# Kernel tuning notes

Hardware: AMD Instinct MI355X
Metric: run time of the kernel (lower is better)

## Reference

```python
import jax, jax.numpy as jnp
import numpy as np

DIM = 96
NUM_HEADS = 6
KSIZE = 3
DILATIONS = (1, 2, 3)
HEAD_DIM = DIM // NUM_HEADS            # 16
NUM_DIL = len(DILATIONS)
GROUP_DIM = DIM // NUM_DIL             # 32 channels per dilation branch
MLP_HIDDEN = int(DIM * 4.0)
SCALE = HEAD_DIM ** -0.5
EPS = 1e-5


def _unfold(x, k, dil):
    """nn.Unfold(k, dilation=dil, padding=dil*(k-1)//2, stride=1).
    x: (B, C, H, W) -> (B, C, k*k, H, W), kernel positions row-major."""
    B, C, H, W = x.shape
    pad = dil * (k - 1) // 2
    xp = jnp.pad(x, ((0, 0), (0, 0), (pad, pad), (pad, pad)))
    pats = [xp[:, :, i * dil:i * dil + H, j * dil:j * dil + W]
            for i in range(k) for j in range(k)]
    return jnp.stack(pats, axis=2)  # (B, C, kk, H, W)


def _layernorm(x, w, b):
    mu = jnp.mean(x, axis=-1, keepdims=True)
    var = jnp.mean(jnp.square(x - mu), axis=-1, keepdims=True)
    return (x - mu) * jax.lax.rsqrt(var + EPS) * w + b


def _dilate_attention(q, k, v, dil):
    """q,k,v: (B, GROUP_DIM, H, W) -> (B, H, W, GROUP_DIM)."""
    B, gd, H, W = q.shape
    h = gd // HEAD_DIM
    kk = KSIZE * KSIZE
    HW = H * W
    qf = q.reshape(B, h, HEAD_DIM, HW)                      # bhdn
    ku = _unfold(k, KSIZE, dil).reshape(B, h, HEAD_DIM, kk, HW)  # bhdkn
    attn = jnp.einsum('bhdn,bhdkn->bhnk', qf, ku) * SCALE   # (B,h,HW,kk)
    attn = jax.nn.softmax(attn, axis=-1)
    vu = _unfold(v, KSIZE, dil).reshape(B, h, HEAD_DIM, kk, HW)
    out = jnp.einsum('bhnk,bhdkn->bnhd', attn, vu)          # (B,HW,h,HEAD_DIM)
    return out.reshape(B, H, W, gd)


def setup_inputs() -> dict:
    key = jax.random.key(0)
    ks = jax.random.split(key, 8)
    B, H, W = 8, 128, 128
    s = 0.02
    return {
        'x': jax.random.normal(ks[0], (B, DIM, H, W), jnp.float32),
        'qkv_w': jax.random.normal(ks[1], (3 * DIM, DIM), jnp.float32) * s,
        'proj_w': jax.random.normal(ks[2], (DIM, DIM), jnp.float32) * s,
        'proj_b': jnp.zeros((DIM,), jnp.float32),
        'ln1_w': jnp.ones((DIM,), jnp.float32),
        'ln1_b': jnp.zeros((DIM,), jnp.float32),
        'ln2_w': jnp.ones((DIM,), jnp.float32),
        'ln2_b': jnp.zeros((DIM,), jnp.float32),
        'fc1_w': jax.random.normal(ks[3], (MLP_HIDDEN, DIM), jnp.float32) * s,
        'fc1_b': jnp.zeros((MLP_HIDDEN,), jnp.float32),
        'fc2_w': jax.random.normal(ks[4], (DIM, MLP_HIDDEN), jnp.float32) * s,
        'fc2_b': jnp.zeros((DIM,), jnp.float32),
    }


def reference(x, qkv_w, proj_w, proj_b, ln1_w, ln1_b, ln2_w, ln2_b,
              fc1_w, fc1_b, fc2_w, fc2_b):
    B, C, H, W = x.shape
    xhw = jnp.transpose(x, (0, 2, 3, 1))                    # (B,H,W,C)

    # --- attention branch ---
    y = _layernorm(xhw, ln1_w, ln1_b)                       # (B,H,W,C)
    # qkv 1x1 conv == per-pixel matmul; output channel layout (3, nd, gd)
    qkv = jnp.einsum('bhwc,oc->bohw', y, qkv_w)             # (B,3C,H,W)
    qkv = qkv.reshape(B, 3, NUM_DIL, GROUP_DIM, H, W)
    outs = [
        _dilate_attention(qkv[:, 0, i], qkv[:, 1, i], qkv[:, 2, i], DILATIONS[i])
        for i in range(NUM_DIL)
    ]
    attn_out = jnp.concatenate(outs, axis=-1)               # (B,H,W,C)
    attn_out = jnp.einsum('bhwc,oc->bhwo', attn_out, proj_w) + proj_b
    xhw = xhw + attn_out

    # --- MLP branch ---
    y = _layernorm(xhw, ln2_w, ln2_b)
    h1 = jax.nn.gelu(jnp.einsum('bhwc,oc->bhwo', y, fc1_w) + fc1_b,
                     approximate=False)
    mlp_out = jnp.einsum('bhwc,oc->bhwo', h1, fc2_w) + fc2_b
    xhw = xhw + mlp_out

    return jnp.transpose(xhw, (0, 3, 1, 2))                 # (B,C,H,W)
```

## Files before the change

### kernel.cpp

```cpp
#include <hip/hip_runtime.h>
#include <hip/hip_bf16.h>
#include <math.h>

typedef __attribute__((ext_vector_type(8))) short bf16x8;
typedef __attribute__((ext_vector_type(4))) float f32x4;
typedef __attribute__((ext_vector_type(2))) unsigned u32x2;

#define MTOT  131072
#define HW16K 16384

__device__ inline float bf2f(unsigned short u) {
    union { unsigned u; float f; } x; x.u = ((unsigned)u) << 16; return x.f;
}
__device__ inline unsigned short f2bf(float a) {
    __hip_bfloat16 h = __float2bfloat16(a);
    union { __hip_bfloat16 h; unsigned short u; } c; c.h = h; return c.u;
}
__device__ inline unsigned pack2bf(float a, float b) {
    __hip_bfloat162 h = __float22bfloat162_rn(make_float2(a, b));
    union { __hip_bfloat162 h; unsigned u; } c; c.h = h; return c.u;
}
__device__ inline float gelu(float v) {
    float u = v * fmaf(0.07135481f, v * v, 1.5957691f);
    return __fdividef(v, 1.f + __expf(-u));
}
__device__ inline void load16(const unsigned short* p, float* f) {
    uint4 u0 = *(const uint4*)p;
    uint4 u1 = *(const uint4*)(p + 8);
    unsigned w[8] = {u0.x, u0.y, u0.z, u0.w, u1.x, u1.y, u1.z, u1.w};
#pragma unroll
    for (int i = 0; i < 8; i++) {
        union { unsigned u; float f; } lo, hi;
        lo.u = w[i] << 16; hi.u = w[i] & 0xffff0000u;
        f[2 * i] = lo.f; f[2 * i + 1] = hi.f;
    }
}

__global__ __launch_bounds__(256) void k_prep(const float* __restrict__ qw,
                                              const float* __restrict__ pw,
                                              const float* __restrict__ f1,
                                              const float* __restrict__ f2,
                                              unsigned short* __restrict__ wq,
                                              unsigned short* __restrict__ wp,
                                              unsigned short* __restrict__ w1t,
                                              unsigned short* __restrict__ w2t) {
    int t = blockIdx.x * 256 + threadIdx.x;
    if (t < 27648) {
        int row = t / 96, col = t - row * 96;
        int s = row / 96;
        int rem = row - s * 96;
        int di = rem >> 5;
        int hd = (rem >> 4) & 1;
        int c  = rem & 15;
        int nrow = s * 96 + (di * 2 + hd) * 16 + c;
        wq[nrow * 96 + col] = f2bf(qw[t]);
    }
    else if (t < 36864) wp[t - 27648] = f2bf(pw[t - 27648]);
    else if (t < 73728) {
        int t2 = t - 36864;
        int och = t2 / 96, col = t2 - och * 96;
        int f  = och >> 5;
        int p  = och & 31;
        int q  = p >> 3, tt = (p >> 2) & 1, r = p & 3;
        int tile = f * 2 + tt;
        int j = q * 4 + r;
        int kf = col >> 5, k = col & 31;
        w1t[((tile * 3 + kf) * 16 + j) * 32 + k] = f2bf(f1[t2]);
    }
    else if (t < 110592) {
        int t3 = t - 73728;
        int row = t3 / 384, col = t3 - row * 384;
        int nt = row >> 4, r = row & 15;
        int kf = col >> 5, k = col & 31;
        w2t[((nt * 12 + kf) * 16 + r) * 32 + k] = f2bf(f2[t3]);
    }
}

__global__ __launch_bounds__(512) void k_ln1qkv(const float* __restrict__ x,
                                                const float* __restrict__ w,
                                                const float* __restrict__ bln,
                                                const unsigned short* __restrict__ wq,
                                                unsigned short* __restrict__ qkvb) {
    __shared__ unsigned short bufbf[256 * 100];
    __shared__ unsigned short Bs[288 * 104];
    __shared__ float ps[512], ps2[512];
    int tid = threadIdx.x;
    int gp0 = blockIdx.x * 256;
    int b = gp0 >> 14, pix0 = gp0 & 16383;
    int p = tid & 255, half = tid >> 8;

    for (int i = tid; i < 3456; i += 512) {
        int row = i / 12, col = i - row * 12;
        *(uint4*)(Bs + row * 104 + col * 8) = ((const uint4*)wq)[i];
    }

    float val[48];
    float s = 0.f, s2 = 0.f;
#pragma unroll
    for (int i = 0; i < 48; i++) {
        int c = half * 48 + i;
        float v = x[((size_t)b * 96 + c) * HW16K + pix0 + p];
        val[i] = v; s += v; s2 += v * v;
    }
    ps[tid] = s; ps2[tid] = s2;
    __syncthreads();
    float st = ps[p] + ps[p + 256];
    float st2 = ps2[p] + ps2[p + 256];
    float mu = st * (1.f / 96.f);
    float inv = rsqrtf(st2 * (1.f / 96.f) - mu * mu + 1e-5f);
#pragma unroll
    for (int i = 0; i < 24; i++) {
        int c = half * 48 + 2 * i;
        float n0 = (val[2 * i] - mu) * inv * w[c] + bln[c];
        float n1 = (val[2 * i + 1] - mu) * inv * w[c + 1] + bln[c + 1];
        *(unsigned*)(bufbf + p * 100 + c) = pack2bf(n0, n1);
    }
    __syncthreads();

    int lane = tid & 63, wv = tid >> 6;
    int q = lane >> 4, l15 = lane & 15;
#pragma unroll 1
    for (int it = 0; it < 2; it++) {
        int pxl = (wv * 2 + it) * 16 + l15;
        bf16x8 pf[3];
#pragma unroll
        for (int f = 0; f < 3; f++)
            pf[f] = *(const bf16x8*)(bufbf + pxl * 100 + q * 8 + f * 32);
        int gpx = gp0 + pxl;
#pragma unroll
        for (int nt = 0; nt < 18; nt++) {
            f32x4 acc = (f32x4){0.f, 0.f, 0.f, 0.f};
#pragma unroll
            for (int f = 0; f < 3; f++) {
                bf16x8 wf = *(const bf16x8*)(Bs + (nt * 16 + l15) * 104 + q * 8 + f * 32);
                acc = __builtin_amdgcn_mfma_f32_16x16x32_bf16(wf, pf[f], acc, 0, 0, 0);
            }
            u32x2 pk = { pack2bf(acc[0], acc[1]), pack2bf(acc[2], acc[3]) };
            __builtin_nontemporal_store(pk,
                (u32x2*)(qkvb + ((size_t)nt * MTOT + gpx) * 16 + q * 4));
        }
    }
}

__global__ __launch_bounds__(256) void k_attn(const unsigned short* __restrict__ qkvb,
                                              unsigned short* __restrict__ attnb) {
    int bid = blockIdx.x;
    int xcd = bid & 7;
    int idx = bid >> 3;
    int g   = idx >> 6;
    int yb  = (xcd << 6) | (idx & 63);
    int px  = yb * 256 + threadIdx.x;

    int d = (g >> 1) + 1;
    int pix = px & 16383;
    int hh = pix >> 7, ww = pix & 127;
    int ibase = px & ~16383;

    const unsigned short* qpl = qkvb + (size_t)g * (MTOT * 16);
    const unsigned short* kpl = qkvb + (size_t)(6 + g) * (MTOT * 16);
    const unsigned short* vpl = qkvb + (size_t)(12 + g) * (MTOT * 16);

    float q[16];
    load16(qpl + (size_t)px * 16, q);

    float sc[9]; int nloc[9]; bool ok[9];
#pragma unroll
    for (int i = 0; i < 3; i++) {
#pragma unroll
        for (int j = 0; j < 3; j++) {
            int k9 = i * 3 + j;
            int yy = hh + (i - 1) * d;
            int xx = ww + (j - 1) * d;
            bool o_ = ((unsigned)yy < 128u) && ((unsigned)xx < 128u);
            ok[k9] = o_;
            nloc[k9] = ibase + yy * 128 + xx;
            float s = 0.f;
            if (o_) {
                float kf[16];
                load16(kpl + (size_t)nloc[k9] * 16, kf);
#pragma unroll
                for (int c = 0; c < 16; c++) s += q[c] * kf[c];
            }
            sc[k9] = s * 0.25f;
        }
    }
    float mx = sc[0];
#pragma unroll
    for (int k9 = 1; k9 < 9; k9++) mx = fmaxf(mx, sc[k9]);
    float sum = 0.f;
#pragma unroll
    for (int k9 = 0; k9 < 9; k9++) { sc[k9] = __expf(sc[k9] - mx); sum += sc[k9]; }
    float rs = 1.f / sum;

    float o[16];
#pragma unroll
    for (int c = 0; c < 16; c++) o[c] = 0.f;
#pragma unroll
    for (int k9 = 0; k9 < 9; k9++) {
        if (ok[k9]) {
            float vf[16];
            load16(vpl + (size_t)nloc[k9] * 16, vf);
            float w9 = sc[k9];
#pragma unroll
            for (int c = 0; c < 16; c++) o[c] += w9 * vf[c];
        }
    }
    uint4* orow = (uint4*)(attnb + ((size_t)g * MTOT + px) * 16);
    uint4 pk0;
    pk0.x = pack2bf(o[0] * rs, o[1] * rs);
    pk0.y = pack2bf(o[2] * rs, o[3] * rs);
    pk0.z = pack2bf(o[4] * rs, o[5] * rs);
    pk0.w = pack2bf(o[6] * rs, o[7] * rs);
    orow[0] = pk0;
    uint4 pk1;
    pk1.x = pack2bf(o[8] * rs, o[9] * rs);
    pk1.y = pack2bf(o[10] * rs, o[11] * rs);
    pk1.z = pack2bf(o[12] * rs, o[13] * rs);
    pk1.w = pack2bf(o[14] * rs, o[15] * rs);
    orow[1] = pk1;
}

__global__ __launch_bounds__(512) void k_projres(const unsigned short* __restrict__ A,
                                                 const unsigned short* __restrict__ Bw,
                                                 const float* __restrict__ bias,
                                                 const float* __restrict__ x,
                                                 const float* __restrict__ lw,
                                                 const float* __restrict__ lb,
                                                 float* __restrict__ x1,
                                                 unsigned short* __restrict__ y2) {
    __shared__ unsigned short Bs[96 * 104];
    int tid = threadIdx.x;
    for (int i = tid; i < 96 * 12; i += 512) {
        int row = i / 12, col = i - row * 12;
        *(uint4*)(Bs + row * 104 + col * 8) = ((const uint4*)Bw)[i];
    }
    __syncthreads();
    int lane = tid & 63, wv = tid >> 6;
    int q = lane >> 4, l15 = lane & 15;

#pragma unroll 1
    for (int it = 0; it < 2; it++) {
        int px = (blockIdx.x * 16 + wv * 2 + it) * 16 + l15;
        bf16x8 pf[3];
#pragma unroll
        for (int f = 0; f < 3; f++) {
            int pa = 2 * f + (q >> 1);
            pf[f] = *(const bf16x8*)(A + ((size_t)pa * MTOT + px) * 16 + (q & 1) * 8);
        }
        f32x4 acc[6];
#pragma unroll
        for (int nt = 0; nt < 6; nt++) acc[nt] = (f32x4){0.f, 0.f, 0.f, 0.f};
#pragma unroll
        for (int nt = 0; nt < 6; nt++) {
            const unsigned short* br = Bs + (nt * 16 + l15) * 104 + q * 8;
#pragma unroll
            for (int f = 0; f < 3; f++) {
                bf16x8 wf = *(const bf16x8*)(br + f * 32);
                acc[nt] = __builtin_amdgcn_mfma_f32_16x16x32_bf16(wf, pf[f], acc[nt], 0, 0, 0);
            }
        }

        int b = px >> 14, pix = px & 16383;
        float v[24];
        float s = 0.f, s2 = 0.f;
#pragma unroll
        for (int nt = 0; nt < 6; nt++) {
            float4 bb = ((const float4*)bias)[nt * 4 + q];
            int och0 = nt * 16 + q * 4;
#pragma unroll
            for (int r = 0; r < 4; r++) {
                float xv = x[((size_t)b * 96 + och0 + r) * HW16K + pix];
                float t = acc[nt][r] + ((&bb.x)[r]) + xv;
                __builtin_nontemporal_store(t, x1 + (size_t)(och0 + r) * MTOT + px);
                v[nt * 4 + r] = t;
                s += t; s2 += t * t;
            }
        }
        s += __shfl_xor(s, 16);  s += __shfl_xor(s, 32);
        s2 += __shfl_xor(s2, 16); s2 += __shfl_xor(s2, 32);
        float mu = s * (1.f / 96.f);
        float inv = rsqrtf(s2 * (1.f / 96.f) - mu * mu + 1e-5f);
#pragma unroll
        for (int nt = 0; nt < 6; nt++) {
            float4 lwv = ((const float4*)lw)[nt * 4 + q];
            float4 lbv = ((const float4*)lb)[nt * 4 + q];
            float n0 = (v[nt * 4 + 0] - mu) * inv * lwv.x + lbv.x;
            float n1 = (v[nt * 4 + 1] - mu) * inv * lwv.y + lbv.y;
            float n2 = (v[nt * 4 + 2] - mu) * inv * lwv.z + lbv.z;
            float n3 = (v[nt * 4 + 3] - mu) * inv * lwv.w + lbv.w;
            uint2 pk;
            pk.x = pack2bf(n0, n1);
            pk.y = pack2bf(n2, n3);
            *(uint2*)(y2 + ((size_t)nt * MTOT + px) * 16 + q * 4) = pk;
        }
    }
}

__global__ __launch_bounds__(256) void k_mlp(const unsigned short* __restrict__ y2,
                                             const unsigned short* __restrict__ w1t,
                                             const float* __restrict__ b1,
                                             const unsigned short* __restrict__ w2t,
                                             const float* __restrict__ b2,
                                             const float* __restrict__ x1,
                                             float* __restrict__ out) {
    int tid = threadIdx.x;
    int lane = tid & 63, wv = tid >> 6;
    int q = lane >> 4, l15 = lane & 15;
    int pt0 = (blockIdx.x * 4 + wv) * 2;
    int px0 = pt0 * 16 + l15;
    int px1 = px0 + 16;

    bf16x8 a0[3], a1[3];
#pragma unroll
    for (int f = 0; f < 3; f++) {
        int pa = 2 * f + (q >> 1);
        a0[f] = *(const bf16x8*)(y2 + ((size_t)pa * MTOT + px0) * 16 + (q & 1) * 8);
        a1[f] = *(const bf16x8*)(y2 + ((size_t)pa * MTOT + px1) * 16 + (q & 1) * 8);
    }

    f32x4 acc2a[6], acc2b[6];
#pragma unroll
    for (int nt = 0; nt < 6; nt++) {
        acc2a[nt] = (f32x4){0.f, 0.f, 0.f, 0.f};
        acc2b[nt] = (f32x4){0.f, 0.f, 0.f, 0.f};
    }

#pragma unroll 1
    for (int f = 0; f < 12; f++) {
        bf16x8 wf0[3], wf1[3];
#pragma unroll
        for (int kf = 0; kf < 3; kf++) {
            wf0[kf] = *(const bf16x8*)(w1t + (((2 * f) * 3 + kf) * 16 + l15) * 32 + q * 8);
            wf1[kf] = *(const bf16x8*)(w1t + (((2 * f + 1) * 3 + kf) * 16 + l15) * 32 + q * 8);
        }
        f32x4 c00 = (f32x4){0.f,0.f,0.f,0.f}, c01 = (f32x4){0.f,0.f,0.f,0.f};
        f32x4 c10 = (f32x4){0.f,0.f,0.f,0.f}, c11 = (f32x4){0.f,0.f,0.f,0.f};
#pragma unroll
        for (int kf = 0; kf < 3; kf++) {
            c00 = __builtin_amdgcn_mfma_f32_16x16x32_bf16(wf0[kf], a0[kf], c00, 0, 0, 0);
            c01 = __builtin_amdgcn_mfma_f32_16x16x32_bf16(wf1[kf], a0[kf], c01, 0, 0, 0);
            c10 = __builtin_amdgcn_mfma_f32_16x16x32_bf16(wf0[kf], a1[kf], c10, 0, 0, 0);
            c11 = __builtin_amdgcn_mfma_f32_16x16x32_bf16(wf1[kf], a1[kf], c11, 0, 0, 0);
        }
        bf16x8 w2f[6];
#pragma unroll
        for (int nt = 0; nt < 6; nt++)
            w2f[nt] = *(const bf16x8*)(w2t + ((nt * 12 + f) * 16 + l15) * 32 + q * 8);

        float4 bb0 = ((const float4*)b1)[8 * f + 2 * q];
        float4 bb1 = ((const float4*)b1)[8 * f + 2 * q + 1];

        union { unsigned u[4]; bf16x8 v; } H0, H1;
        H0.u[0] = pack2bf(gelu(c00[0] + bb0.x), gelu(c00[1] + bb0.y));
        H0.u[1] = pack2bf(gelu(c00[2] + bb0.z), gelu(c00[3] + bb0.w));
        H0.u[2] = pack2bf(gelu(c01[0] + bb1.x), gelu(c01[1] + bb1.y));
        H0.u[3] = pack2bf(gelu(c01[2] + bb1.z), gelu(c01[3] + bb1.w));
        H1.u[0] = pack2bf(gelu(c10[0] + bb0.x), gelu(c10[1] + bb0.y));
        H1.u[1] = pack2bf(gelu(c10[2] + bb0.z), gelu(c10[3] + bb0.w));
        H1.u[2] = pack2bf(gelu(c11[0] + bb1.x), gelu(c11[1] + bb1.y));
        H1.u[3] = pack2bf(gelu(c11[2] + bb1.z), gelu(c11[3] + bb1.w));

#pragma unroll
        for (int nt = 0; nt < 6; nt++) {
            acc2a[nt] = __builtin_amdgcn_mfma_f32_16x16x32_bf16(w2f[nt], H0.v, acc2a[nt], 0, 0, 0);
            acc2b[nt] = __builtin_amdgcn_mfma_f32_16x16x32_bf16(w2f[nt], H1.v, acc2b[nt], 0, 0, 0);
        }
    }

    int b0 = px0 >> 14, pia = px0 & 16383;
    int b1i = px1 >> 14, pib = px1 & 16383;
#pragma unroll
    for (int nt = 0; nt < 6; nt++) {
        float4 bb = ((const float4*)b2)[nt * 4 + q];
        int och0 = nt * 16 + q * 4;
#pragma unroll
        for (int r = 0; r < 4; r++) {
            float ov0 = acc2a[nt][r] + ((&bb.x)[r]) + x1[(size_t)(och0 + r) * MTOT + px0];
            __builtin_nontemporal_store(ov0, out + ((size_t)b0 * 96 + och0 + r) * HW16K + pia);
            float ov1 = acc2b[nt][r] + ((&bb.x)[r]) + x1[(size_t)(och0 + r) * MTOT + px1];
            __builtin_nontemporal_store(ov1, out + ((size_t)b1i * 96 + och0 + r) * HW16K + pib);
        }
    }
}

extern "C" void kernel_launch(void* const* d_in, const int* in_sizes, int n_in,
                              void* d_out, int out_size, void* d_ws, size_t ws_size,
                              hipStream_t stream) {
    const float* x      = (const float*)d_in[0];
    const float* qkv_w  = (const float*)d_in[1];
    const float* proj_w = (const float*)d_in[2];
    const float* proj_b = (const float*)d_in[3];
    const float* ln1w   = (const float*)d_in[4];
    const float* ln1b   = (const float*)d_in[5];
    const float* ln2w   = (const float*)d_in[6];
    const float* ln2b   = (const float*)d_in[7];
    const float* fc1w   = (const float*)d_in[8];
    const float* fc1b   = (const float*)d_in[9];
    const float* fc2w   = (const float*)d_in[10];
    const float* fc2b   = (const float*)d_in[11];
    float* out = (float*)d_out;

    char* ws = (char*)d_ws;
    unsigned short* wq  = (unsigned short*)(ws);
    unsigned short* wp  = (unsigned short*)(ws + 55296);
    unsigned short* w1t = (unsigned short*)(ws + 73728);
    unsigned short* w2t = (unsigned short*)(ws + 147456);
    unsigned short* rA   = (unsigned short*)(ws + 221184);
    unsigned short* qkvb = (unsigned short*)(ws + 25387008);
    float*          x1   = (float*)(ws + 25387008);
    unsigned short* y2   = (unsigned short*)(ws + 25387008 + 50331648);

    k_prep<<<432, 256, 0, stream>>>(qkv_w, proj_w, fc1w, fc2w, wq, wp, w1t, w2t);

    k_ln1qkv<<<512, 512, 0, stream>>>(x, ln1w, ln1b, wq, qkvb);
    k_attn<<<3072, 256, 0, stream>>>(qkvb, rA);
    k_projres<<<512, 512, 0, stream>>>(rA, wp, proj_b, x, ln2w, ln2b, x1, y2);
    k_mlp<<<1024, 256, 0, stream>>>(y2, w1t, fc1b, w2t, fc2b, x1, out);
}
```

Baseline: 267.4 us.

## Fuse projection, residual, LayerNorm2 and MLP into one kernel

```diff
diff --git a/kernel.cpp b/kernel.cpp
--- a/kernel.cpp
+++ b/kernel.cpp
@@ -40,10 +40,15 @@
                                               const float* __restrict__ pw,
                                               const float* __restrict__ f1,
                                               const float* __restrict__ f2,
+                                              const float* __restrict__ pb,
+                                              const float* __restrict__ l2w,
+                                              const float* __restrict__ l2b,
+                                              const float* __restrict__ f2b,
                                               unsigned short* __restrict__ wq,
-                                              unsigned short* __restrict__ wp,
+                                              unsigned short* __restrict__ wpt,
                                               unsigned short* __restrict__ w1t,
-                                              unsigned short* __restrict__ w2t) {
+                                              unsigned short* __restrict__ w2t,
+                                              float* __restrict__ scal) {
     int t = blockIdx.x * 256 + threadIdx.x;
     if (t < 27648) {
         int row = t / 96, col = t - row * 96;
@@ -55,7 +60,13 @@
         int nrow = s * 96 + (di * 2 + hd) * 16 + c;
         wq[nrow * 96 + col] = f2bf(qw[t]);
     }
-    else if (t < 36864) wp[t - 27648] = f2bf(pw[t - 27648]);
+    else if (t < 36864) {
+        int t2 = t - 27648;
+        int och = t2 / 96, ich = t2 - och * 96;
+        int nt = ((och >> 5) << 1) + ((och >> 2) & 1);
+        int j  = ((och >> 3) & 3) * 4 + (och & 3);
+        wpt[((nt * 3 + (ich >> 5)) * 16 + j) * 32 + (ich & 31)] = f2bf(pw[t2]);
+    }
     else if (t < 73728) {
         int t2 = t - 36864;
         int och = t2 / 96, col = t2 - och * 96;
@@ -64,15 +75,22 @@
         int q  = p >> 3, tt = (p >> 2) & 1, r = p & 3;
         int tile = f * 2 + tt;
         int j = q * 4 + r;
-        int kf = col >> 5, k = col & 31;
-        w1t[((tile * 3 + kf) * 16 + j) * 32 + k] = f2bf(f1[t2]);
+        w1t[((tile * 3 + (col >> 5)) * 16 + j) * 32 + (col & 31)] = f2bf(f1[t2]);
     }
     else if (t < 110592) {
         int t3 = t - 73728;
-        int row = t3 / 384, col = t3 - row * 384;
-        int nt = row >> 4, r = row & 15;
-        int kf = col >> 5, k = col & 31;
-        w2t[((nt * 12 + kf) * 16 + r) * 32 + k] = f2bf(f2[t3]);
+        int och = t3 / 384, ich = t3 - och * 384;
+        int nt = ((och >> 5) << 1) + ((och >> 2) & 1);
+        int j  = ((och >> 3) & 3) * 4 + (och & 3);
+        w2t[((nt * 12 + (ich >> 5)) * 16 + j) * 32 + (ich & 31)] = f2bf(f2[t3]);
+    }
+    else if (t < 110976) {
+        int i = t - 110592;
+        int s = i / 96, slot = i - s * 96;
+        int nt = slot >> 4, qq = (slot >> 2) & 3, r = slot & 3;
+        int c = ((nt >> 1) << 5) + qq * 8 + ((nt & 1) << 2) + r;
+        const float* src = (s == 0) ? pb : (s == 1) ? l2w : (s == 2) ? l2b : f2b;
+        scal[i] = src[c];
     }
 }
 
@@ -220,89 +238,14 @@
     orow[1] = pk1;
 }
 
-__global__ __launch_bounds__(512) void k_projres(const unsigned short* __restrict__ A,
-                                                 const unsigned short* __restrict__ Bw,
-                                                 const float* __restrict__ bias,
-                                                 const float* __restrict__ x,
-                                                 const float* __restrict__ lw,
-                                                 const float* __restrict__ lb,
-                                                 float* __restrict__ x1,
-                                                 unsigned short* __restrict__ y2) {
-    __shared__ unsigned short Bs[96 * 104];
-    int tid = threadIdx.x;
-    for (int i = tid; i < 96 * 12; i += 512) {
-        int row = i / 12, col = i - row * 12;
-        *(uint4*)(Bs + row * 104 + col * 8) = ((const uint4*)Bw)[i];
-    }
-    __syncthreads();
-    int lane = tid & 63, wv = tid >> 6;
-    int q = lane >> 4, l15 = lane & 15;
-
-#pragma unroll 1
-    for (int it = 0; it < 2; it++) {
-        int px = (blockIdx.x * 16 + wv * 2 + it) * 16 + l15;
-        bf16x8 pf[3];
-#pragma unroll
-        for (int f = 0; f < 3; f++) {
-            int pa = 2 * f + (q >> 1);
-            pf[f] = *(const bf16x8*)(A + ((size_t)pa * MTOT + px) * 16 + (q & 1) * 8);
-        }
-        f32x4 acc[6];
-#pragma unroll
-        for (int nt = 0; nt < 6; nt++) acc[nt] = (f32x4){0.f, 0.f, 0.f, 0.f};
-#pragma unroll
-        for (int nt = 0; nt < 6; nt++) {
-            const unsigned short* br = Bs + (nt * 16 + l15) * 104 + q * 8;
-#pragma unroll
-            for (int f = 0; f < 3; f++) {
-                bf16x8 wf = *(const bf16x8*)(br + f * 32);
-                acc[nt] = __builtin_amdgcn_mfma_f32_16x16x32_bf16(wf, pf[f], acc[nt], 0, 0, 0);
-            }
-        }
-
-        int b = px >> 14, pix = px & 16383;
-        float v[24];
-        float s = 0.f, s2 = 0.f;
-#pragma unroll
-        for (int nt = 0; nt < 6; nt++) {
-            float4 bb = ((const float4*)bias)[nt * 4 + q];
-            int och0 = nt * 16 + q * 4;
-#pragma unroll
-            for (int r = 0; r < 4; r++) {
-                float xv = x[((size_t)b * 96 + och0 + r) * HW16K + pix];
-                float t = acc[nt][r] + ((&bb.x)[r]) + xv;
-                __builtin_nontemporal_store(t, x1 + (size_t)(och0 + r) * MTOT + px);
-                v[nt * 4 + r] = t;
-                s += t; s2 += t * t;
-            }
-        }
-        s += __shfl_xor(s, 16);  s += __shfl_xor(s, 32);
-        s2 += __shfl_xor(s2, 16); s2 += __shfl_xor(s2, 32);
-        float mu = s * (1.f / 96.f);
-        float inv = rsqrtf(s2 * (1.f / 96.f) - mu * mu + 1e-5f);
-#pragma unroll
-        for (int nt = 0; nt < 6; nt++) {
-            float4 lwv = ((const float4*)lw)[nt * 4 + q];
-            float4 lbv = ((const float4*)lb)[nt * 4 + q];
-            float n0 = (v[nt * 4 + 0] - mu) * inv * lwv.x + lbv.x;
-            float n1 = (v[nt * 4 + 1] - mu) * inv * lwv.y + lbv.y;
-            float n2 = (v[nt * 4 + 2] - mu) * inv * lwv.z + lbv.z;
-            float n3 = (v[nt * 4 + 3] - mu) * inv * lwv.w + lbv.w;
-            uint2 pk;
-            pk.x = pack2bf(n0, n1);
-            pk.y = pack2bf(n2, n3);
-            *(uint2*)(y2 + ((size_t)nt * MTOT + px) * 16 + q * 4) = pk;
-        }
-    }
-}
-
-__global__ __launch_bounds__(256) void k_mlp(const unsigned short* __restrict__ y2,
-                                             const unsigned short* __restrict__ w1t,
-                                             const float* __restrict__ b1,
-                                             const unsigned short* __restrict__ w2t,
-                                             const float* __restrict__ b2,
-                                             const float* __restrict__ x1,
-                                             float* __restrict__ out) {
+__global__ __launch_bounds__(256) void k_pmlp(const unsigned short* __restrict__ attnb,
+                                              const unsigned short* __restrict__ wpt,
+                                              const float* __restrict__ scal,
+                                              const float* __restrict__ x,
+                                              const unsigned short* __restrict__ w1t,
+                                              const float* __restrict__ b1,
+                                              const unsigned short* __restrict__ w2t,
+                                              float* __restrict__ out) {
     int tid = threadIdx.x;
     int lane = tid & 63, wv = tid >> 6;
     int q = lane >> 4, l15 = lane & 15;
@@ -310,13 +253,68 @@
     int px0 = pt0 * 16 + l15;
     int px1 = px0 + 16;
 
+    float v0[24], v1[24];
     bf16x8 a0[3], a1[3];
-#pragma unroll
-    for (int f = 0; f < 3; f++) {
-        int pa = 2 * f + (q >> 1);
-        a0[f] = *(const bf16x8*)(y2 + ((size_t)pa * MTOT + px0) * 16 + (q & 1) * 8);
-        a1[f] = *(const bf16x8*)(y2 + ((size_t)pa * MTOT + px1) * 16 + (q & 1) * 8);
-    }
+
+#define PROJ_TILE(PX, V, A)                                                      \
+    do {                                                                         \
+        bf16x8 pf[3];                                                            \
+        _Pragma("unroll")                                                        \
+        for (int f = 0; f < 3; f++) {                                            \
+            int pa = 2 * f + (q >> 1);                                           \
+            pf[f] = *(const bf16x8*)(attnb + ((size_t)pa * MTOT + (PX)) * 16 + (q & 1) * 8); \
+        }                                                                        \
+        f32x4 acc[6];                                                            \
+        _Pragma("unroll")                                                        \
+        for (int nt = 0; nt < 6; nt++) acc[nt] = (f32x4){0.f, 0.f, 0.f, 0.f};    \
+        _Pragma("unroll")                                                        \
+        for (int nt = 0; nt < 6; nt++) {                                         \
+            _Pragma("unroll")                                                    \
+            for (int kf = 0; kf < 3; kf++) {                                     \
+                bf16x8 wf = *(const bf16x8*)(wpt + ((nt * 3 + kf) * 16 + l15) * 32 + q * 8); \
+                acc[nt] = __builtin_amdgcn_mfma_f32_16x16x32_bf16(wf, pf[kf], acc[nt], 0, 0, 0); \
+            }                                                                    \
+        }                                                                        \
+        int bb_ = (PX) >> 14, pix_ = (PX) & 16383;                               \
+        float s_ = 0.f, s2_ = 0.f;                                               \
+        _Pragma("unroll")                                                        \
+        for (int nt = 0; nt < 6; nt++) {                                         \
+            float4 pbq = ((const float4*)scal)[nt * 4 + q];                      \
+            int cb = ((nt >> 1) << 5) + q * 8 + ((nt & 1) << 2);                 \
+            _Pragma("unroll")                                                    \
+            for (int r = 0; r < 4; r++) {                                        \
+                float xv = x[((size_t)bb_ * 96 + cb + r) * HW16K + pix_];        \
+                float t_ = acc[nt][r] + ((&pbq.x)[r]) + xv;                      \
+                V[nt * 4 + r] = t_; s_ += t_; s2_ += t_ * t_;                    \
+            }                                                                    \
+        }                                                                        \
+        s_ += __shfl_xor(s_, 16);  s_ += __shfl_xor(s_, 32);                     \
+        s2_ += __shfl_xor(s2_, 16); s2_ += __shfl_xor(s2_, 32);                  \
+        float mu_ = s_ * (1.f / 96.f);                                           \
+        float inv_ = rsqrtf(s2_ * (1.f / 96.f) - mu_ * mu_ + 1e-5f);             \
+        float nrm[24];                                                           \
+        _Pragma("unroll")                                                        \
+        for (int nt = 0; nt < 6; nt++) {                                         \
+            float4 lwq = ((const float4*)(scal + 96))[nt * 4 + q];               \
+            float4 lbq = ((const float4*)(scal + 192))[nt * 4 + q];              \
+            _Pragma("unroll")                                                    \
+            for (int r = 0; r < 4; r++)                                          \
+                nrm[nt * 4 + r] = (V[nt * 4 + r] - mu_) * inv_ * ((&lwq.x)[r]) + ((&lbq.x)[r]); \
+        }                                                                        \
+        _Pragma("unroll")                                                        \
+        for (int kf = 0; kf < 3; kf++) {                                         \
+            union { unsigned u[4]; bf16x8 v; } Hh;                               \
+            Hh.u[0] = pack2bf(nrm[(kf * 2) * 4 + 0], nrm[(kf * 2) * 4 + 1]);     \
+            Hh.u[1] = pack2bf(nrm[(kf * 2) * 4 + 2], nrm[(kf * 2) * 4 + 3]);     \
+            Hh.u[2] = pack2bf(nrm[(kf * 2 + 1) * 4 + 0], nrm[(kf * 2 + 1) * 4 + 1]); \
+            Hh.u[3] = pack2bf(nrm[(kf * 2 + 1) * 4 + 2], nrm[(kf * 2 + 1) * 4 + 3]); \
+            A[kf] = Hh.v;                                                        \
+        }                                                                        \
+    } while (0)
+
+    PROJ_TILE(px0, v0, a0);
+    PROJ_TILE(px1, v1, a1);
+#undef PROJ_TILE
 
     f32x4 acc2a[6], acc2b[6];
 #pragma unroll
@@ -349,7 +347,6 @@
 
         float4 bb0 = ((const float4*)b1)[8 * f + 2 * q];
         float4 bb1 = ((const float4*)b1)[8 * f + 2 * q + 1];
-
         union { unsigned u[4]; bf16x8 v; } H0, H1;
         H0.u[0] = pack2bf(gelu(c00[0] + bb0.x), gelu(c00[1] + bb0.y));
         H0.u[1] = pack2bf(gelu(c00[2] + bb0.z), gelu(c00[3] + bb0.w));
@@ -371,14 +368,14 @@
     int b1i = px1 >> 14, pib = px1 & 16383;
 #pragma unroll
     for (int nt = 0; nt < 6; nt++) {
-        float4 bb = ((const float4*)b2)[nt * 4 + q];
-        int och0 = nt * 16 + q * 4;
+        float4 b2q = ((const float4*)(scal + 288))[nt * 4 + q];
+        int cb = ((nt >> 1) << 5) + q * 8 + ((nt & 1) << 2);
 #pragma unroll
         for (int r = 0; r < 4; r++) {
-            float ov0 = acc2a[nt][r] + ((&bb.x)[r]) + x1[(size_t)(och0 + r) * MTOT + px0];
-            __builtin_nontemporal_store(ov0, out + ((size_t)b0 * 96 + och0 + r) * HW16K + pia);
-            float ov1 = acc2b[nt][r] + ((&bb.x)[r]) + x1[(size_t)(och0 + r) * MTOT + px1];
-            __builtin_nontemporal_store(ov1, out + ((size_t)b1i * 96 + och0 + r) * HW16K + pib);
+            float ov0 = acc2a[nt][r] + ((&b2q.x)[r]) + v0[nt * 4 + r];
+            __builtin_nontemporal_store(ov0, out + ((size_t)b0 * 96 + cb + r) * HW16K + pia);
+            float ov1 = acc2b[nt][r] + ((&b2q.x)[r]) + v1[nt * 4 + r];
+            __builtin_nontemporal_store(ov1, out + ((size_t)b1i * 96 + cb + r) * HW16K + pib);
         }
     }
 }
@@ -401,19 +398,19 @@
     float* out = (float*)d_out;
 
     char* ws = (char*)d_ws;
-    unsigned short* wq  = (unsigned short*)(ws);
-    unsigned short* wp  = (unsigned short*)(ws + 55296);
-    unsigned short* w1t = (unsigned short*)(ws + 73728);
-    unsigned short* w2t = (unsigned short*)(ws + 147456);
-    unsigned short* rA   = (unsigned short*)(ws + 221184);
-    unsigned short* qkvb = (unsigned short*)(ws + 25387008);
-    float*          x1   = (float*)(ws + 25387008);
-    unsigned short* y2   = (unsigned short*)(ws + 25387008 + 50331648);
-
-    k_prep<<<432, 256, 0, stream>>>(qkv_w, proj_w, fc1w, fc2w, wq, wp, w1t, w2t);
+    unsigned short* wq   = (unsigned short*)(ws);
+    unsigned short* wpt  = (unsigned short*)(ws + 55296);
+    unsigned short* w1t  = (unsigned short*)(ws + 73728);
+    unsigned short* w2t  = (unsigned short*)(ws + 147456);
+    float*          scal = (float*)(ws + 221184);
+    unsigned short* rA   = (unsigned short*)(ws + 230400);
+    unsigned short* qkvb = (unsigned short*)(ws + 25396224);
+
+    k_prep<<<434, 256, 0, stream>>>(qkv_w, proj_w, fc1w, fc2w,
+                                    proj_b, ln2w, ln2b, fc2b,
+                                    wq, wpt, w1t, w2t, scal);
 
     k_ln1qkv<<<512, 512, 0, stream>>>(x, ln1w, ln1b, wq, qkvb);
     k_attn<<<3072, 256, 0, stream>>>(qkvb, rA);
-    k_projres<<<512, 512, 0, stream>>>(rA, wp, proj_b, x, ln2w, ln2b, x1, y2);
-    k_mlp<<<1024, 256, 0, stream>>>(y2, w1t, fc1b, w2t, fc2b, x1, out);
-}
+    k_pmlp<<<1024, 256, 0, stream>>>(rA, wpt, scal, x, w1t, fc1b, w2t, out);
+}
```

Measured after the change: 238.8 us, median of 2. 10.7% less time.
